# Optimization experiments

Measured on AMD Instinct MI355X. Metric: run time of the kernel, lower is better.

Reference implementation:

```python
import jax, jax.numpy as jnp
import numpy as np

B, C, H, W = 16, 1, 128, 8192
N_MAX = 128
CHIRP_W, PERIOD = 48, 64
W_OUT = N_MAX * CHIRP_W + (N_MAX - 1)  # 6271 compacted columns (chirps + separators)
SEP_CLASS_ID = 2


def setup_inputs() -> dict:
    key = jax.random.key(0)
    k1, k2, k3, k4 = jax.random.split(key, 4)
    x = jax.random.normal(k1, (B, C, H, W), dtype=jnp.float32)
    starts = jnp.arange(N_MAX, dtype=jnp.int32) * PERIOD
    xi = jnp.stack([starts, starts + CHIRP_W], axis=-1)           # (N_MAX, 2)
    xi = jnp.broadcast_to(xi[None], (B, N_MAX, 2)).astype(jnp.int32)
    N = jax.random.randint(k2, (B,), 96, N_MAX + 1, dtype=jnp.int32)
    N = N.at[0].set(N_MAX)  # pin so static W_OUT equals torch's dynamic int(w_max.max())
    xl = jax.random.randint(k3, (B, W), 0, 2, dtype=jnp.int32)
    sep_param = jax.random.normal(k4, (1, 1, 1), dtype=jnp.float32)
    return {"x": x, "xi": xi, "N": N, "xl": xl, "sep_param": sep_param, "w_out": W_OUT}


def _compactify(x, xi, N, xl, sep_param, w_out):
    """Vectorized TinyBird.compactify_data: remove silence, keep chirp blocks,
    insert one separator column between consecutive valid chirps."""
    Bx, Cx, Hx, Wx = x.shape
    n_max = xi.shape[1]
    idx = jnp.arange(n_max, dtype=jnp.int32)[None, :]             # (1, N_max)
    Nb = N.reshape(-1, 1).astype(jnp.int32)
    valid = idx < Nb                                              # (B, N_max)

    s0, e0 = xi[..., 0], xi[..., 1]
    w = jnp.clip(e0 - s0, 0, None)
    w_valid = jnp.where(valid, w, 0)
    csum = jnp.cumsum(w_valid, axis=1)
    sn = csum - w_valid + idx                                     # new start (seps before = idx)
    en = csum + idx                                               # new end
    xi_new = jnp.where(valid[..., None], jnp.stack([sn, en], -1), 0).astype(xi.dtype)

    BIG = jnp.int32(1 << 30)
    en_srt = jnp.where(valid, en, BIG)                            # strictly increasing over valid part
    t = jnp.arange(w_out, dtype=jnp.int32)[None, :]               # (1, w_out)
    # i = number of chirp ends <= t  ->  chirp whose [sn_i, en_i) may contain t
    i = (en_srt[:, :, None] <= t[:, None, :]).sum(axis=1).astype(jnp.int32)  # (B, w_out)
    ic = jnp.clip(i, 0, n_max - 1)
    take = lambda a: jnp.take_along_axis(a, ic, axis=1)
    sn_i, en_i = take(sn), take(en)
    s0_i, e0_i = take(s0), take(e0)
    in_chirp = (i < Nb) & (t >= sn_i) & (en_i > sn_i) & (e0_i > s0_i)
    src = jnp.clip(s0_i + (t - sn_i), 0, Wx - 1)                  # (B, w_out)

    # separator column: t == en_{i-1}, previous chirp is not the last valid one, en < W
    jp = jnp.clip(i - 1, 0, n_max - 1)
    en_prev = jnp.take_along_axis(en, jp, axis=1)
    is_sep = (i >= 1) & (t == en_prev) & ((i - 1) < (Nb - 1)) & (en_prev < Wx)

    x_g = jnp.take_along_axis(x, src[:, None, None, :], axis=3)   # (B, C, H, w_out)
    sep = sep_param[0, 0, 0]
    x_new = jnp.where(in_chirp[:, None, None, :], x_g,
                      jnp.where(is_sep[:, None, None, :], sep, jnp.float32(0)))
    xl_g = jnp.take_along_axis(xl, src, axis=1)
    xl_new = jnp.where(in_chirp, xl_g,
                       jnp.where(is_sep, jnp.asarray(SEP_CLASS_ID, xl.dtype),
                                 jnp.asarray(0, xl.dtype)))
    return x_new, xi_new, xl_new


def reference(x, xi, N, xl, sep_param, w_out):
    return _compactify(x, xi, N, xl, sep_param, w_out)
```

## Files before the change

kernel.cpp:

```cpp
#include <hip/hip_runtime.h>

#define BB     16
#define HH     128
#define WW     8192
#define N_MAXC 128
#define W_OUTC 6271
#define SEP_CLASS 2.0f

#define X_ELEMS (BB * HH * W_OUTC)
#define XI_OFF  (X_ELEMS)
#define XL_OFF  (X_ELEMS + BB * N_MAXC * 2)

#define TCOLS 512
#define HROWS 16
#define NTILE 13

typedef int vi4 __attribute__((ext_vector_type(4)));

__global__ __launch_bounds__(256, 4) void tb_fused(const float* __restrict__ x,
                                                   const int* __restrict__ xi,
                                                   const int* __restrict__ Nv,
                                                   const int* __restrict__ xl,
                                                   const float* __restrict__ sep_param,
                                                   float* __restrict__ out) {
    __shared__ int s_s0[N_MAXC], s_e0[N_MAXC], s_scan[N_MAXC], s_sn[N_MAXC], s_en[N_MAXC];
    __shared__ __align__(16) int s_map[TCOLS];

    const int t0  = blockIdx.x * TCOLS;
    const int h0  = blockIdx.y * HROWS;
    const int b   = blockIdx.z;
    const int tid = threadIdx.x;
    const int Nb  = Nv[b];

    int wv = 0;
    if (tid < N_MAXC) {
        int2 se = ((const int2*)xi)[b * N_MAXC + tid];
        s_s0[tid] = se.x; s_e0[tid] = se.y;
        int w = se.y - se.x; if (w < 0) w = 0;
        wv = (tid < Nb) ? w : 0;
        s_scan[tid] = wv;
    }
    __syncthreads();
    #pragma unroll
    for (int off = 1; off < N_MAXC; off <<= 1) {
        int v = 0;
        if (tid < N_MAXC && tid >= off) v = s_scan[tid - off];
        __syncthreads();
        if (tid < N_MAXC) s_scan[tid] += v;
        __syncthreads();
    }
    if (tid < N_MAXC) {
        int c = s_scan[tid];
        s_sn[tid] = c - wv + tid;
        s_en[tid] = c + tid;
    }
    __syncthreads();

    #pragma unroll
    for (int q = 0; q < 2; ++q) {
        const int j = tid + q * 256;
        const int t = t0 + j;
        int m = -2;
        if (t < W_OUTC) {
            int lo = 0, hi = Nb;
            while (lo < hi) { int mid = (lo + hi) >> 1; if (s_en[mid] <= t) lo = mid + 1; else hi = mid; }
            const int i  = lo;
            const int ic = (i < N_MAXC - 1) ? i : (N_MAXC - 1);
            if (i < Nb) {
                int sn = s_sn[ic], en = s_en[ic];
                if (t >= sn && en > sn && s_e0[ic] > s_s0[ic]) {
                    int src = s_s0[ic] + (t - sn);
                    m = src < 0 ? 0 : (src > WW - 1 ? WW - 1 : src);
                }
            }
            if (m == -2 && i >= 1) {
                int ep = s_en[i - 1];
                if (t == ep && (i - 1) < (Nb - 1) && ep < WW) m = -1;
            }
        }
        s_map[j] = m;
    }

    if (blockIdx.y == 0 && blockIdx.x == 0 && tid < N_MAXC) {
        const bool valid = tid < Nb;
        out[XI_OFF + (b * N_MAXC + tid) * 2 + 0] = valid ? (float)s_sn[tid] : 0.0f;
        out[XI_OFF + (b * N_MAXC + tid) * 2 + 1] = valid ? (float)s_en[tid] : 0.0f;
    }
    __syncthreads();

    if (blockIdx.y == 0) {
        #pragma unroll
        for (int q = 0; q < 2; ++q) {
            const int j = tid + q * 256;
            const int t = t0 + j;
            if (t < W_OUTC) {
                const int m = s_map[j];
                float v = (m >= 0) ? (float)xl[b * WW + m] : ((m == -1) ? SEP_CLASS : 0.0f);
                out[XL_OFF + b * W_OUTC + t] = v;
            }
        }
    }

    const float sep = sep_param[0];
    const int   c   = tid & 127;
    const int   rb  = tid >> 7;
    const vi4   mv  = ((const vi4*)s_map)[c];
    const int   tA  = t0 + 4 * c;

    const float* xb = x   + ((size_t)b << 20);
    float*       ob = out + (size_t)b * (HH * W_OUTC);

    const unsigned a0 = (mv.x >= 0) ? (unsigned)mv.x : 0u;
    const unsigned a1 = (mv.y >= 0) ? (unsigned)mv.y : 0u;
    const unsigned a2 = (mv.z >= 0) ? (unsigned)mv.z : 0u;
    const unsigned a3 = (mv.w >= 0) ? (unsigned)mv.w : 0u;
    const float f0 = (mv.x == -1) ? sep : 0.0f;
    const float f1 = (mv.y == -1) ? sep : 0.0f;
    const float f2 = (mv.z == -1) ? sep : 0.0f;
    const float f3 = (mv.w == -1) ? sep : 0.0f;

    if (tA + 3 < W_OUTC) {
        #pragma unroll
        for (int rr = 0; rr < HROWS / 2; ++rr) {
            const int h = h0 + rb + rr * 2;
            const float* xr = xb + ((size_t)h << 13);
            float* orow = ob + (size_t)h * W_OUTC + tA;
            const float v0 = (mv.x >= 0) ? xr[a0] : f0;
            const float v1 = (mv.y >= 0) ? xr[a1] : f1;
            const float v2 = (mv.z >= 0) ? xr[a2] : f2;
            const float v3 = (mv.w >= 0) ? xr[a3] : f3;
            orow[0] = v0; orow[1] = v1; orow[2] = v2; orow[3] = v3;
        }
    } else if (tA < W_OUTC) {
        const int nrem = W_OUTC - tA;
        #pragma unroll
        for (int rr = 0; rr < HROWS / 2; ++rr) {
            const int h = h0 + rb + rr * 2;
            const float* xr = xb + ((size_t)h << 13);
            float* orow = ob + (size_t)h * W_OUTC + tA;
            if (nrem > 0) orow[0] = (mv.x >= 0) ? xr[a0] : f0;
            if (nrem > 1) orow[1] = (mv.y >= 0) ? xr[a1] : f1;
            if (nrem > 2) orow[2] = (mv.z >= 0) ? xr[a2] : f2;
        }
    }
}

extern "C" void kernel_launch(void* const* d_in, const int* in_sizes, int n_in,
                              void* d_out, int out_size, void* d_ws, size_t ws_size,
                              hipStream_t stream) {
    const float* x   = (const float*)d_in[0];
    const int*   xi  = (const int*)  d_in[1];
    const int*   Nv  = (const int*)  d_in[2];
    const int*   xl  = (const int*)  d_in[3];
    const float* sep = (const float*)d_in[4];
    float*       out = (float*)d_out;

    dim3 grid(NTILE, HH / HROWS, BB);
    tb_fused<<<grid, dim3(256), 0, stream>>>(x, xi, Nv, xl, sep, out);
}
```

Before: 126.1 us.

## Split prefix scan into separate kernel and vectorize gather with fast contiguous path

Moves the per-batch prefix scan into a small kernel that writes chirp start/end positions to workspace, so each gather block only loads them instead of recomputing the scan with many barriers. The gather kernel checks whether a thread's four output columns fall entirely inside one chirp and, if so, copies them with a single unaligned 4-wide load and store per row. Columns outside that case use the per-column mapping. This adds a second launch and a workspace dependency, and keeps the old fused kernel as a fallback when no workspace is given.

```diff
diff --git a/kernel.cpp b/kernel.cpp
--- a/kernel.cpp
+++ b/kernel.cpp
@@ -14,8 +14,145 @@
 #define TCOLS 512
 #define HROWS 16
 #define NTILE 13
-
-typedef int vi4 __attribute__((ext_vector_type(4)));
+#define WS_INTS (BB * 2 * N_MAXC)
+
+typedef float vf4u __attribute__((ext_vector_type(4), aligned(4)));
+typedef int   vi4  __attribute__((ext_vector_type(4)));
+
+__device__ __forceinline__ int map_col_lds(int t, int Nb,
+                                           const int* s_s0, const int* s_e0,
+                                           const int* s_sn, const int* s_en) {
+    int lo = 0, hi = Nb;
+    while (lo < hi) { int mid = (lo + hi) >> 1; if (s_en[mid] <= t) lo = mid + 1; else hi = mid; }
+    const int i  = lo;
+    const int ic = (i < N_MAXC - 1) ? i : (N_MAXC - 1);
+    if (i < Nb) {
+        int sn = s_sn[ic], en = s_en[ic];
+        if (t >= sn && en > sn && s_e0[ic] > s_s0[ic]) {
+            int src = s_s0[ic] + (t - sn);
+            return src < 0 ? 0 : (src > WW - 1 ? WW - 1 : src);
+        }
+    }
+    if (i >= 1) {
+        int ep = s_en[i - 1];
+        if (t == ep && (i - 1) < (Nb - 1) && ep < WW) return -1;
+    }
+    return -2;
+}
+
+__global__ __launch_bounds__(128) void tb_scan(const int* __restrict__ xi,
+                                               const int* __restrict__ Nv,
+                                               float* __restrict__ out,
+                                               int* __restrict__ ws) {
+    __shared__ int s_scan[N_MAXC];
+    const int b   = blockIdx.x;
+    const int tid = threadIdx.x;
+    const int Nb  = Nv[b];
+    int2 se = ((const int2*)xi)[b * N_MAXC + tid];
+    int w = se.y - se.x; if (w < 0) w = 0;
+    const int wv = (tid < Nb) ? w : 0;
+    s_scan[tid] = wv;
+    __syncthreads();
+    #pragma unroll
+    for (int off = 1; off < N_MAXC; off <<= 1) {
+        int v = (tid >= off) ? s_scan[tid - off] : 0;
+        __syncthreads();
+        s_scan[tid] += v;
+        __syncthreads();
+    }
+    const int c  = s_scan[tid];
+    const int sn = c - wv + tid;
+    const int en = c + tid;
+    ws[b * 2 * N_MAXC + tid]          = sn;
+    ws[b * 2 * N_MAXC + N_MAXC + tid] = en;
+    const bool valid = tid < Nb;
+    out[XI_OFF + (b * N_MAXC + tid) * 2 + 0] = valid ? (float)sn : 0.0f;
+    out[XI_OFF + (b * N_MAXC + tid) * 2 + 1] = valid ? (float)en : 0.0f;
+}
+
+__global__ __launch_bounds__(256) void tb_gather(const float* __restrict__ x,
+                                                 const int* __restrict__ xi,
+                                                 const int* __restrict__ Nv,
+                                                 const int* __restrict__ xl,
+                                                 const float* __restrict__ sep_param,
+                                                 const int* __restrict__ ws,
+                                                 float* __restrict__ out) {
+    __shared__ int s_sn[N_MAXC], s_en[N_MAXC], s_s0[N_MAXC], s_e0[N_MAXC];
+    const int t0  = blockIdx.x * TCOLS;
+    const int h0  = blockIdx.y * HROWS;
+    const int b   = blockIdx.z;
+    const int tid = threadIdx.x;
+    const int Nb  = Nv[b];
+
+    if (tid < N_MAXC) {
+        s_sn[tid] = ws[b * 2 * N_MAXC + tid];
+        s_en[tid] = ws[b * 2 * N_MAXC + N_MAXC + tid];
+        int2 se = ((const int2*)xi)[b * N_MAXC + tid];
+        s_s0[tid] = se.x; s_e0[tid] = se.y;
+    }
+    __syncthreads();
+
+    const float sep = sep_param[0];
+    const float* xb = x   + ((size_t)b << 20);
+    float*       ob = out + (size_t)b * (HH * (size_t)W_OUTC);
+
+    if (blockIdx.y == 0) {
+        #pragma unroll
+        for (int q = 0; q < 2; ++q) {
+            const int t = t0 + tid + q * 256;
+            if (t < W_OUTC) {
+                const int m = map_col_lds(t, Nb, s_s0, s_e0, s_sn, s_en);
+                float v = (m >= 0) ? (float)xl[b * WW + m] : ((m == -1) ? SEP_CLASS : 0.0f);
+                out[XL_OFF + b * W_OUTC + t] = v;
+            }
+        }
+    }
+
+    const int c  = tid & 127;
+    const int rb = tid >> 7;
+    const int tA = t0 + 4 * c;
+
+    int lo = 0, hi = Nb;
+    while (lo < hi) { int mid = (lo + hi) >> 1; if (s_en[mid] <= tA) lo = mid + 1; else hi = mid; }
+    const int i = lo;
+    bool fast = false; int src = 0;
+    if (tA + 3 < W_OUTC && i < Nb) {
+        const int sn = s_sn[i], en = s_en[i];
+        if (tA >= sn && tA + 3 < en && s_e0[i] > s_s0[i]) {
+            fast = true;
+            src  = s_s0[i] + (tA - sn);
+        }
+    }
+
+    if (fast) {
+        #pragma unroll
+        for (int rr = 0; rr < HROWS / 2; ++rr) {
+            const int h = h0 + rb + rr * 2;
+            const vf4u v = *(const vf4u*)(xb + ((size_t)h << 13) + src);
+            *(vf4u*)(ob + (size_t)h * W_OUTC + tA) = v;
+        }
+    } else {
+        int m[4];
+        #pragma unroll
+        for (int kk = 0; kk < 4; ++kk) {
+            const int t = tA + kk;
+            m[kk] = (t < W_OUTC) ? map_col_lds(t, Nb, s_s0, s_e0, s_sn, s_en) : -3;
+        }
+        #pragma unroll
+        for (int rr = 0; rr < HROWS / 2; ++rr) {
+            const int h = h0 + rb + rr * 2;
+            const float* xr   = xb + ((size_t)h << 13);
+            float*       orow = ob + (size_t)h * W_OUTC;
+            #pragma unroll
+            for (int kk = 0; kk < 4; ++kk) {
+                const int mm = m[kk];
+                if (mm != -3) {
+                    orow[tA + kk] = (mm >= 0) ? xr[mm] : ((mm == -1) ? sep : 0.0f);
+                }
+            }
+        }
+    }
+}
 
 __global__ __launch_bounds__(256, 4) void tb_fused(const float* __restrict__ x,
                                                    const int* __restrict__ xi,
@@ -25,13 +162,11 @@
                                                    float* __restrict__ out) {
     __shared__ int s_s0[N_MAXC], s_e0[N_MAXC], s_scan[N_MAXC], s_sn[N_MAXC], s_en[N_MAXC];
     __shared__ __align__(16) int s_map[TCOLS];
-
     const int t0  = blockIdx.x * TCOLS;
     const int h0  = blockIdx.y * HROWS;
     const int b   = blockIdx.z;
     const int tid = threadIdx.x;
     const int Nb  = Nv[b];
-
     int wv = 0;
     if (tid < N_MAXC) {
         int2 se = ((const int2*)xi)[b * N_MAXC + tid];
@@ -55,39 +190,18 @@
         s_en[tid] = c + tid;
     }
     __syncthreads();
-
     #pragma unroll
     for (int q = 0; q < 2; ++q) {
         const int j = tid + q * 256;
         const int t = t0 + j;
-        int m = -2;
-        if (t < W_OUTC) {
-            int lo = 0, hi = Nb;
-            while (lo < hi) { int mid = (lo + hi) >> 1; if (s_en[mid] <= t) lo = mid + 1; else hi = mid; }
-            const int i  = lo;
-            const int ic = (i < N_MAXC - 1) ? i : (N_MAXC - 1);
-            if (i < Nb) {
-                int sn = s_sn[ic], en = s_en[ic];
-                if (t >= sn && en > sn && s_e0[ic] > s_s0[ic]) {
-                    int src = s_s0[ic] + (t - sn);
-                    m = src < 0 ? 0 : (src > WW - 1 ? WW - 1 : src);
-                }
-            }
-            if (m == -2 && i >= 1) {
-                int ep = s_en[i - 1];
-                if (t == ep && (i - 1) < (Nb - 1) && ep < WW) m = -1;
-            }
-        }
-        s_map[j] = m;
-    }
-
+        s_map[j] = (t < W_OUTC) ? map_col_lds(t, Nb, s_s0, s_e0, s_sn, s_en) : -2;
+    }
     if (blockIdx.y == 0 && blockIdx.x == 0 && tid < N_MAXC) {
         const bool valid = tid < Nb;
         out[XI_OFF + (b * N_MAXC + tid) * 2 + 0] = valid ? (float)s_sn[tid] : 0.0f;
         out[XI_OFF + (b * N_MAXC + tid) * 2 + 1] = valid ? (float)s_en[tid] : 0.0f;
     }
     __syncthreads();
-
     if (blockIdx.y == 0) {
         #pragma unroll
         for (int q = 0; q < 2; ++q) {
@@ -100,16 +214,13 @@
             }
         }
     }
-
     const float sep = sep_param[0];
     const int   c   = tid & 127;
     const int   rb  = tid >> 7;
     const vi4   mv  = ((const vi4*)s_map)[c];
     const int   tA  = t0 + 4 * c;
-
     const float* xb = x   + ((size_t)b << 20);
     float*       ob = out + (size_t)b * (HH * W_OUTC);
-
     const unsigned a0 = (mv.x >= 0) ? (unsigned)mv.x : 0u;
     const unsigned a1 = (mv.y >= 0) ? (unsigned)mv.y : 0u;
     const unsigned a2 = (mv.z >= 0) ? (unsigned)mv.z : 0u;
@@ -118,7 +229,6 @@
     const float f1 = (mv.y == -1) ? sep : 0.0f;
     const float f2 = (mv.z == -1) ? sep : 0.0f;
     const float f3 = (mv.w == -1) ? sep : 0.0f;
-
     if (tA + 3 < W_OUTC) {
         #pragma unroll
         for (int rr = 0; rr < HROWS / 2; ++rr) {
@@ -156,5 +266,12 @@
     float*       out = (float*)d_out;
 
     dim3 grid(NTILE, HH / HROWS, BB);
-    tb_fused<<<grid, dim3(256), 0, stream>>>(x, xi, Nv, xl, sep, out);
-}
+
+    if (d_ws && ws_size >= WS_INTS * sizeof(int)) {
+        int* ws = (int*)d_ws;
+        tb_scan<<<dim3(BB), dim3(128), 0, stream>>>(xi, Nv, out, ws);
+        tb_gather<<<grid, dim3(256), 0, stream>>>(x, xi, Nv, xl, sep, ws, out);
+    } else {
+        tb_fused<<<grid, dim3(256), 0, stream>>>(x, xi, Nv, xl, sep, out);
+    }
+}
```

Result: slower. 140.7 us (+11.6%).
